# Performance work log

Measured on AMD Instinct MI355X. Metric: run time of the kernel, lower is better.

## Reference

```python
import jax, jax.numpy as jnp
import numpy as np

B, IN_SIZE, IN_DIM = 16, 2048, 512
HEADS, OUT_SIZE = 4, 64
EPS = 0.1
MAX_ITER = 30
SIGMA = 0.1


def setup_inputs() -> dict:
    key = jax.random.key(0)
    k1, k2 = jax.random.split(key)
    x = jax.random.normal(k1, (B, IN_SIZE, IN_DIM), dtype=jnp.float32)
    stdv = 1.0 / np.sqrt(OUT_SIZE)
    weight = jax.random.uniform(k2, (HEADS, OUT_SIZE, IN_DIM), jnp.float32, -stdv, stdv)
    return {"x": x, "weight": weight}


def _position_filter(in_size, out_size, sigma):
    # 1-D gaussian position filter (image=False branch of get_position_filter)
    a = jnp.arange(0.0, in_size, dtype=jnp.float32)[:, None] / in_size
    b = jnp.arange(0.0, out_size, dtype=jnp.float32)[None, :] / out_size
    return jnp.exp(-(((a - b) / sigma) ** 2))  # (in_size, out_size)


def log_sinkhorn(K, iterations):
    """Log-domain Sinkhorn. K: (B, H, N, M) log-kernel.
    Row marginal a = 1/N (uniform, no mask). Scaling vectors are
    detached (envelope trick) before forming the transport plan,
    matching the original OTK implementation."""
    Bn, H, N, M = K.shape
    log_a = jnp.full((Bn, H, N), -jnp.log(jnp.float32(N)), dtype=K.dtype)
    u0 = jnp.zeros((Bn, H, N), K.dtype)
    v0 = jnp.zeros((Bn, H, M), K.dtype)

    def step(carry, _):
        u, v = carry
        Z = K + u[..., :, None] + v[..., None, :]
        u = log_a - jax.nn.logsumexp(Z, axis=-1)
        Z = K + u[..., :, None] + v[..., None, :]
        v = -jax.nn.logsumexp(Z, axis=-2)
        return (u, v), None

    (u, v), _ = jax.lax.scan(step, (u0, v0), None, length=iterations)
    u = jax.lax.stop_gradient(u)
    v = jax.lax.stop_gradient(v)
    return jnp.exp(K + u[..., :, None] + v[..., None, :])  # (B,H,N,M)


def reference(x, weight):
    # x: (B, N, D); weight: (H, M, D)
    pf = _position_filter(IN_SIZE, OUT_SIZE, SIGMA)  # (N, M)
    # euclidean cost via expansion (cdist)
    x2 = jnp.sum(x * x, axis=-1)                      # (B, N)
    w2 = jnp.sum(weight * weight, axis=-1)            # (H, M)
    xw = jnp.einsum('bnd,hmd->bhnm', x, weight)       # (B, H, N, M)
    C = jnp.sqrt(jnp.maximum(x2[:, None, :, None] + w2[None, :, None, :] - 2.0 * xw, 0.0))
    K = (-C / EPS) * pf[None, None]                   # position filter applied to log-kernel
    P = log_sinkhorn(K, MAX_ITER)                     # (B, H, N, M) transport plan
    # attn: (B, M, H, N) -> (B, M*H, N)
    attn = jnp.transpose(P, (0, 3, 1, 2)).reshape(B, OUT_SIZE * HEADS, IN_SIZE)
    out = jnp.matmul(attn, x)                         # (B, M*H, D)
    return out.reshape(B, OUT_SIZE, HEADS * IN_DIM)
```

## Files before the change

### kernel.cpp

```cpp
#include <hip/hip_runtime.h>
#include <hip/hip_fp16.h>


typedef _Float16 h2 __attribute__((ext_vector_type(2)));
typedef _Float16 h8 __attribute__((ext_vector_type(8)));
typedef float f4 __attribute__((ext_vector_type(4)));

#define NB 16
#define NN 2048
#define ND 512
#define NH 4
#define NM 64
#define NITER 30
#define EUSCALE 8.0f

static __device__ __forceinline__ float fdot2f(h2 a, h2 b, float c) {
#if __has_builtin(__builtin_amdgcn_fdot2)
  return __builtin_amdgcn_fdot2(a, b, c, false);
#else
  return (float)a[0] * (float)b[0] + (float)a[1] * (float)b[1] + c;
#endif
}

static __device__ __forceinline__ h2 pkrtz(float a, float b) {
  return __builtin_bit_cast(h2, __builtin_amdgcn_cvt_pkrtz(a, b));
}

static __device__ __forceinline__ h8 pack8(float4 a, float4 b) {
  h8 r;
  r[0] = (_Float16)a.x; r[1] = (_Float16)a.y; r[2] = (_Float16)a.z; r[3] = (_Float16)a.w;
  r[4] = (_Float16)b.x; r[5] = (_Float16)b.y; r[6] = (_Float16)b.z; r[7] = (_Float16)b.w;
  return r;
}

static __device__ __forceinline__ float sq4(float4 a) {
  return a.x * a.x + a.y * a.y + a.z * a.z + a.w * a.w;
}

__global__ __launch_bounds__(256) void k0_xt(const float* __restrict__ x,
                                             _Float16* __restrict__ xT) {
  __shared__ float tile[64][65];
  const int b = blockIdx.z;
  const int n0 = blockIdx.x * 64;
  const int d0 = blockIdx.y * 64;
  const int t = threadIdx.x;
  const int nr = t >> 2;
  const int ds = (t & 3) * 16;
  const float4* src = (const float4*)(x + ((size_t)(b * NN + n0 + nr) * ND + d0 + ds));
  float4 v0 = src[0], v1 = src[1], v2 = src[2], v3 = src[3];
  float vals[16] = {v0.x, v0.y, v0.z, v0.w, v1.x, v1.y, v1.z, v1.w,
                    v2.x, v2.y, v2.z, v2.w, v3.x, v3.y, v3.z, v3.w};
#pragma unroll
  for (int j = 0; j < 16; ++j) tile[ds + j][nr] = vals[j];
  __syncthreads();
  const int dr = t >> 2;
  const int ns = (t & 3) * 16;
  h8 o0, o1;
#pragma unroll
  for (int j = 0; j < 8; ++j) o0[j] = (_Float16)tile[dr][ns + j];
#pragma unroll
  for (int j = 0; j < 8; ++j) o1[j] = (_Float16)tile[dr][ns + 8 + j];
  _Float16* dst = xT + ((size_t)(b * ND + d0 + dr) * NN + n0 + ns);
  *(h8*)dst = o0;
  *(h8*)(dst + 8) = o1;
}

__global__ __launch_bounds__(512) void k1_buildE(const float* __restrict__ x,
                                                 const float* __restrict__ w,
                                                 _Float16* __restrict__ E) {
  __shared__ _Float16 Ah[128][72];
  __shared__ _Float16 Bh[256][72];
  __shared__ float x2s[128][4];
  __shared__ float w2s[256][2];
  __shared__ float x2r[128];
  __shared__ float w2r[256];

  const int b = blockIdx.y;
  const int n0 = blockIdx.x * 128;
  const int tid = threadIdx.x;
  const int lane = tid & 63;
  const int wv = tid >> 6;
  const int lrow = lane & 15;
  const int kq = lane >> 4;

  f4 acc[16];
#pragma unroll
  for (int i = 0; i < 16; ++i) acc[i] = (f4){0.f, 0.f, 0.f, 0.f};

  const int ar = tid >> 2, ac = (tid & 3) * 16;
  const int br = tid >> 1, bc = (tid & 1) * 32;
  const float* xsrc = x + ((size_t)(b * NN + n0 + ar) * ND + ac);
  const float* wsrc = w + ((size_t)br * ND + bc);
  float x2p = 0.f, w2p = 0.f;

  for (int kt = 0; kt < 8; ++kt) {
    {
      const float4* s4 = (const float4*)(xsrc + kt * 64);
      float4 a0 = s4[0], a1 = s4[1], a2 = s4[2], a3 = s4[3];
      x2p += sq4(a0) + sq4(a1) + sq4(a2) + sq4(a3);
      *(h8*)&Ah[ar][ac] = pack8(a0, a1);
      *(h8*)&Ah[ar][ac + 8] = pack8(a2, a3);
    }
    {
      const float4* s4 = (const float4*)(wsrc + kt * 64);
      float4 u0 = s4[0], u1 = s4[1], u2 = s4[2], u3 = s4[3];
      float4 u4 = s4[4], u5 = s4[5], u6 = s4[6], u7 = s4[7];
      w2p += sq4(u0) + sq4(u1) + sq4(u2) + sq4(u3)
           + sq4(u4) + sq4(u5) + sq4(u6) + sq4(u7);
      *(h8*)&Bh[br][bc] = pack8(u0, u1);
      *(h8*)&Bh[br][bc + 8] = pack8(u2, u3);
      *(h8*)&Bh[br][bc + 16] = pack8(u4, u5);
      *(h8*)&Bh[br][bc + 24] = pack8(u6, u7);
    }
    __syncthreads();
#pragma unroll
    for (int s = 0; s < 2; ++s) {
      h8 af = *(const h8*)&Ah[wv * 16 + lrow][s * 32 + kq * 8];
#pragma unroll
      for (int cf = 0; cf < 16; ++cf) {
        h8 bf = *(const h8*)&Bh[cf * 16 + lrow][s * 32 + kq * 8];
        acc[cf] = __builtin_amdgcn_mfma_f32_16x16x32_f16(af, bf, acc[cf], 0, 0, 0);
      }
    }
    __syncthreads();
  }

  x2s[ar][tid & 3] = x2p;
  w2s[br][tid & 1] = w2p;
  __syncthreads();
  if (tid < 128) {
    x2r[tid] = x2s[tid][0] + x2s[tid][1] + x2s[tid][2] + x2s[tid][3];
  } else if (tid < 384) {
    const int r = tid - 128;
    w2r[r] = w2s[r][0] + w2s[r][1];
  }
  __syncthreads();

#pragma unroll
  for (int cf = 0; cf < 16; ++cf) {
    const int mg = cf * 16 + lrow;
    const int hh = mg >> 6;
    const int m = mg & 63;
    const float w2v = w2r[mg];
    const float bm = (float)m * (1.0f / 64.0f);
    _Float16* Eb = E + ((size_t)(b * NH + hh) * NN) * NM;
#pragma unroll
    for (int j = 0; j < 4; ++j) {
      const int nl = wv * 16 + kq * 4 + j;
      const int n = n0 + nl;
      const float c2 = x2r[nl] + w2v - 2.0f * acc[cf][j];
      const float Cd = sqrtf(fmaxf(c2, 0.0f));
      const float tt = (float)n * (1.0f / 2048.0f) - bm;
      const float pf = __expf(-100.0f * tt * tt);
      const float Ev = __expf(-10.0f * Cd * pf);
      Eb[(size_t)n * NM + m] = (_Float16)Ev;
    }
  }
}

__global__ __launch_bounds__(1024) void k2_sinkhorn(const _Float16* __restrict__ E,
                                                    _Float16* __restrict__ Pt) {
  const int bh = blockIdx.x;
  const int b = bh >> 2, h = bh & 3;
  const int tid = threadIdx.x;
  const int lane = tid & 63;

  __shared__ float evf[64];
  __shared__ __align__(16) h2 evh[32];
  __shared__ unsigned int pbuf[1024];

  const _Float16* Ep = E + (size_t)bh * (NN * NM);

  h2 e[2][32];
#pragma unroll
  for (int i = 0; i < 2; ++i) {
    const uint4* src = (const uint4*)(Ep + (size_t)(2 * tid + i) * NM);
#pragma unroll
    for (int q = 0; q < 8; ++q) {
      uint4 v = src[q];
      e[i][q * 4 + 0] = __builtin_bit_cast(h2, v.x);
      e[i][q * 4 + 1] = __builtin_bit_cast(h2, v.y);
      e[i][q * 4 + 2] = __builtin_bit_cast(h2, v.z);
      e[i][q * 4 + 3] = __builtin_bit_cast(h2, v.w);
    }
  }

  float eu[2] = {1.f, 1.f};
  if (tid < 64) evf[tid] = 1.f;
  if (tid < 32) evh[tid] = pkrtz(1.f, 1.f);
  __syncthreads();

#pragma unroll 1
  for (int it = 0; it < NITER; ++it) {
    h2 evr[32];
    {
      const uint4* ev4 = (const uint4*)evh;
#pragma unroll
      for (int q8 = 0; q8 < 8; ++q8) {
        uint4 v = ev4[q8];
        evr[q8 * 4 + 0] = __builtin_bit_cast(h2, v.x);
        evr[q8 * 4 + 1] = __builtin_bit_cast(h2, v.y);
        evr[q8 * 4 + 2] = __builtin_bit_cast(h2, v.z);
        evr[q8 * 4 + 3] = __builtin_bit_cast(h2, v.w);
      }
    }
    float s0a = 0.f, s0b = 0.f, s1a = 0.f, s1b = 0.f;
#pragma unroll
    for (int q = 0; q < 16; ++q) {
      s0a = fdot2f(e[0][q], evr[q], s0a);
      s1a = fdot2f(e[1][q], evr[q], s1a);
    }
#pragma unroll
    for (int q = 16; q < 32; ++q) {
      s0b = fdot2f(e[0][q], evr[q], s0b);
      s1b = fdot2f(e[1][q], evr[q], s1b);
    }
    eu[0] = 4.8828125e-4f * __builtin_amdgcn_rcpf(eu[0] * (s0a + s0b));
    eu[1] = 4.8828125e-4f * __builtin_amdgcn_rcpf(eu[1] * (s1a + s1b));
    const float es0 = eu[0] * EUSCALE, es1 = eu[1] * EUSCALE;
    const h2 eup0 = pkrtz(es0, es0);
    const h2 eup1 = pkrtz(es1, es1);
    h2 tp[32];
#pragma unroll
    for (int q = 0; q < 32; ++q) {
      tp[q] = e[0][q] * eup0 + e[1][q] * eup1;
    }
#pragma unroll
    for (int k = 0; k < 5; ++k) {
      const int nn = 32 >> k;
      const bool up = (lane >> k) & 1;
#pragma unroll
      for (int p = 0; p < (nn >> 1); ++p) {
        h2 keep = up ? tp[p + (nn >> 1)] : tp[p];
        h2 send = up ? tp[p] : tp[p + (nn >> 1)];
        int rv = __shfl_xor(__builtin_bit_cast(int, send), 1 << k, 64);
        tp[p] = keep + __builtin_bit_cast(h2, rv);
      }
    }
    pbuf[tid] = __builtin_bit_cast(unsigned int, tp[0]);
    __syncthreads();
    if (tid < 32) {
      const int j = tid;
      const int rev = ((j & 1) << 4) | ((j & 2) << 2) | (j & 4) | ((j & 8) >> 2) | ((j & 16) >> 4);
      float T0 = 0.f, T1 = 0.f;
#pragma unroll
      for (int wq = 0; wq < 16; ++wq) {
        h2 a = __builtin_bit_cast(h2, pbuf[wq * 64 + rev]);
        h2 c = __builtin_bit_cast(h2, pbuf[wq * 64 + rev + 32]);
        T0 += (float)a[0] + (float)c[0];
        T1 += (float)a[1] + (float)c[1];
      }
      const float e0 = evf[2 * j], e1 = evf[2 * j + 1];
      const float n0 = EUSCALE * __builtin_amdgcn_rcpf(e0 * T0);
      const float n1 = EUSCALE * __builtin_amdgcn_rcpf(e1 * T1);
      evf[2 * j] = n0;
      evf[2 * j + 1] = n1;
      evh[j] = pkrtz(n0, n1);
    }
    __syncthreads();
  }

  _Float16* Pb = Pt + ((size_t)(b * 256 + h)) * NN;
#pragma unroll
  for (int q = 0; q < 32; ++q) {
    const float ev0 = evf[2 * q];
    const float ev1 = evf[2 * q + 1];
    const float a00 = (float)e[0][q][0] * eu[0] * ev0;
    const float a10 = (float)e[1][q][0] * eu[1] * ev0;
    const float a01 = (float)e[0][q][1] * eu[0] * ev1;
    const float a11 = (float)e[1][q][1] * eu[1] * ev1;
    *(h2*)(Pb + (size_t)(2 * q) * 4 * NN + 2 * tid) = pkrtz(a00, a10);
    *(h2*)(Pb + (size_t)(2 * q + 1) * 4 * NN + 2 * tid) = pkrtz(a01, a11);
  }
}

__global__ __launch_bounds__(512) void k3_out(const _Float16* __restrict__ Pt,
                                              const _Float16* __restrict__ xT,
                                              float* __restrict__ out) {
  __shared__ _Float16 As[128][72];
  __shared__ _Float16 Bs[64][72];
  const int b = blockIdx.z;
  const int hf = blockIdx.y;
  const int dt = blockIdx.x;
  const int tid = threadIdx.x;
  const int lane = tid & 63;
  const int wv = tid >> 6;
  const int lrow = lane & 15;
  const int kq = lane >> 4;

  f4 acc[4];
#pragma unroll
  for (int i = 0; i < 4; ++i) acc[i] = (f4){0.f, 0.f, 0.f, 0.f};

  const int ar = tid >> 2, ac = (tid & 3) * 16;
  const int brd = tid >> 3, bn = (tid & 7) * 8;
  const _Float16* asrc = Pt + ((size_t)(b * 256 + hf * 128 + ar) * NN + ac);
  const _Float16* bsrc = xT + ((size_t)(b * ND + dt * 64 + brd) * NN + bn);

  for (int kt = 0; kt < 32; ++kt) {
    const int k0 = kt * 64;
    h8 a0 = *(const h8*)(asrc + k0);
    h8 a1 = *(const h8*)(asrc + k0 + 8);
    h8 bv = *(const h8*)(bsrc + k0);
    *(h8*)&As[ar][ac] = a0;
    *(h8*)&As[ar][ac + 8] = a1;
    *(h8*)&Bs[brd][bn] = bv;
    __syncthreads();
#pragma unroll
    for (int s = 0; s < 2; ++s) {
      h8 af = *(const h8*)&As[wv * 16 + lrow][s * 32 + kq * 8];
#pragma unroll
      for (int cf = 0; cf < 4; ++cf) {
        h8 bf = *(const h8*)&Bs[cf * 16 + lrow][s * 32 + kq * 8];
        acc[cf] = __builtin_amdgcn_mfma_f32_16x16x32_f16(af, bf, acc[cf], 0, 0, 0);
      }
    }
    __syncthreads();
  }
#pragma unroll
  for (int cf = 0; cf < 4; ++cf) {
    const int d = dt * 64 + cf * 16 + lrow;
#pragma unroll
    for (int j = 0; j < 4; ++j) {
      const int row = hf * 128 + wv * 16 + kq * 4 + j;
      out[(size_t)(b * 256 + row) * ND + d] = acc[cf][j];
    }
  }
}

extern "C" void kernel_launch(void* const* d_in, const int* in_sizes, int n_in,
                              void* d_out, int out_size, void* d_ws, size_t ws_size,
                              hipStream_t stream) {
  const float* x = (const float*)d_in[0];
  const float* w = (const float*)d_in[1];
  float* out = (float*)d_out;
  char* ws = (char*)d_ws;
  _Float16* xT = (_Float16*)ws;
  _Float16* E  = (_Float16*)(ws + (size_t)33554432);
  _Float16* Pt = (_Float16*)(ws + (size_t)50331648);

  k0_xt<<<dim3(32, 8, NB), 256, 0, stream>>>(x, xT);
  k1_buildE<<<dim3(16, NB), 512, 0, stream>>>(x, w, E);
  k2_sinkhorn<<<dim3(64), 1024, 0, stream>>>(E, Pt);
  k3_out<<<dim3(8, 2, NB), 512, 0, stream>>>(Pt, xT, out);
}
```

Before: 184.5 us.

## Halve sinkhorn block to 512 threads with four register-pinned rows each

The Sinkhorn kernel now runs 512 threads per block, each holding four rows of E (128 packed half2 registers) instead of two, and all storage is in named scalars pinned with empty asm so it stays in VGPRs. Column partial sums are combined over 8 waves instead of 16, and the epilogue writes 8-byte stores. This cuts cross-wave reduction and shuffle traffic per row, but raises register pressure and gives less latency hiding per block.

After: 178.1 us. 1.04x faster.

```diff
diff --git a/kernel.cpp b/kernel.cpp
--- a/kernel.cpp
+++ b/kernel.cpp
@@ -158,8 +158,23 @@
   }
 }
 
-__global__ __launch_bounds__(1024) void k2_sinkhorn(const _Float16* __restrict__ E,
-                                                    _Float16* __restrict__ Pt) {
+#define H2C(v, c) __builtin_bit_cast(h2, (v).c)
+#define EH(i, j, c) __builtin_bit_cast(h2, E##i##_##j##c)
+
+#define E_LIST(X) \
+  X(0,0) X(0,1) X(0,2) X(0,3) X(0,4) X(0,5) X(0,6) X(0,7) \
+  X(1,0) X(1,1) X(1,2) X(1,3) X(1,4) X(1,5) X(1,6) X(1,7) \
+  X(2,0) X(2,1) X(2,2) X(2,3) X(2,4) X(2,5) X(2,6) X(2,7) \
+  X(3,0) X(3,1) X(3,2) X(3,3) X(3,4) X(3,5) X(3,6) X(3,7)
+
+#define TP_LIST(X) \
+  X(0,0,x)  X(1,0,y)  X(2,0,z)  X(3,0,w)  X(4,1,x)  X(5,1,y)  X(6,1,z)  X(7,1,w) \
+  X(8,2,x)  X(9,2,y)  X(10,2,z) X(11,2,w) X(12,3,x) X(13,3,y) X(14,3,z) X(15,3,w) \
+  X(16,4,x) X(17,4,y) X(18,4,z) X(19,4,w) X(20,5,x) X(21,5,y) X(22,5,z) X(23,5,w) \
+  X(24,6,x) X(25,6,y) X(26,6,z) X(27,6,w) X(28,7,x) X(29,7,y) X(30,7,z) X(31,7,w)
+
+__global__ __launch_bounds__(512, 2) void k2_sinkhorn(const _Float16* __restrict__ E,
+                                                      _Float16* __restrict__ Pt) {
   const int bh = blockIdx.x;
   const int b = bh >> 2, h = bh & 3;
   const int tid = threadIdx.x;
@@ -167,84 +182,91 @@
 
   __shared__ float evf[64];
   __shared__ __align__(16) h2 evh[32];
-  __shared__ unsigned int pbuf[1024];
+  __shared__ unsigned int pbuf[512];
 
   const _Float16* Ep = E + (size_t)bh * (NN * NM);
-
-  h2 e[2][32];
-#pragma unroll
-  for (int i = 0; i < 2; ++i) {
-    const uint4* src = (const uint4*)(Ep + (size_t)(2 * tid + i) * NM);
-#pragma unroll
-    for (int q = 0; q < 8; ++q) {
-      uint4 v = src[q];
-      e[i][q * 4 + 0] = __builtin_bit_cast(h2, v.x);
-      e[i][q * 4 + 1] = __builtin_bit_cast(h2, v.y);
-      e[i][q * 4 + 2] = __builtin_bit_cast(h2, v.z);
-      e[i][q * 4 + 3] = __builtin_bit_cast(h2, v.w);
-    }
-  }
-
-  float eu[2] = {1.f, 1.f};
+  const uint4* s0 = (const uint4*)(Ep + (size_t)(4 * tid + 0) * NM);
+  const uint4* s1 = (const uint4*)(Ep + (size_t)(4 * tid + 1) * NM);
+  const uint4* s2 = (const uint4*)(Ep + (size_t)(4 * tid + 2) * NM);
+  const uint4* s3 = (const uint4*)(Ep + (size_t)(4 * tid + 3) * NM);
+
+#define DECLE(i, j) \
+  uint4 v##i##_##j = s##i[j]; \
+  unsigned int E##i##_##j##x = v##i##_##j.x; \
+  unsigned int E##i##_##j##y = v##i##_##j.y; \
+  unsigned int E##i##_##j##z = v##i##_##j.z; \
+  unsigned int E##i##_##j##w = v##i##_##j.w;
+  E_LIST(DECLE)
+#undef DECLE
+#define PINE(i, j) \
+  asm volatile("" : "+v"(E##i##_##j##x), "+v"(E##i##_##j##y), \
+                    "+v"(E##i##_##j##z), "+v"(E##i##_##j##w));
+  E_LIST(PINE)
+#undef PINE
+
+  float eu0 = 1.f, eu1 = 1.f, eu2 = 1.f, eu3 = 1.f;
   if (tid < 64) evf[tid] = 1.f;
   if (tid < 32) evh[tid] = pkrtz(1.f, 1.f);
   __syncthreads();
 
 #pragma unroll 1
   for (int it = 0; it < NITER; ++it) {
-    h2 evr[32];
-    {
-      const uint4* ev4 = (const uint4*)evh;
-#pragma unroll
-      for (int q8 = 0; q8 < 8; ++q8) {
-        uint4 v = ev4[q8];
-        evr[q8 * 4 + 0] = __builtin_bit_cast(h2, v.x);
-        evr[q8 * 4 + 1] = __builtin_bit_cast(h2, v.y);
-        evr[q8 * 4 + 2] = __builtin_bit_cast(h2, v.z);
-        evr[q8 * 4 + 3] = __builtin_bit_cast(h2, v.w);
-      }
-    }
-    float s0a = 0.f, s0b = 0.f, s1a = 0.f, s1b = 0.f;
-#pragma unroll
-    for (int q = 0; q < 16; ++q) {
-      s0a = fdot2f(e[0][q], evr[q], s0a);
-      s1a = fdot2f(e[1][q], evr[q], s1a);
-    }
-#pragma unroll
-    for (int q = 16; q < 32; ++q) {
-      s0b = fdot2f(e[0][q], evr[q], s0b);
-      s1b = fdot2f(e[1][q], evr[q], s1b);
-    }
-    eu[0] = 4.8828125e-4f * __builtin_amdgcn_rcpf(eu[0] * (s0a + s0b));
-    eu[1] = 4.8828125e-4f * __builtin_amdgcn_rcpf(eu[1] * (s1a + s1b));
-    const float es0 = eu[0] * EUSCALE, es1 = eu[1] * EUSCALE;
-    const h2 eup0 = pkrtz(es0, es0);
-    const h2 eup1 = pkrtz(es1, es1);
-    h2 tp[32];
-#pragma unroll
-    for (int q = 0; q < 32; ++q) {
-      tp[q] = e[0][q] * eup0 + e[1][q] * eup1;
-    }
-#pragma unroll
-    for (int k = 0; k < 5; ++k) {
-      const int nn = 32 >> k;
-      const bool up = (lane >> k) & 1;
-#pragma unroll
-      for (int p = 0; p < (nn >> 1); ++p) {
-        h2 keep = up ? tp[p + (nn >> 1)] : tp[p];
-        h2 send = up ? tp[p] : tp[p + (nn >> 1)];
-        int rv = __shfl_xor(__builtin_bit_cast(int, send), 1 << k, 64);
-        tp[p] = keep + __builtin_bit_cast(h2, rv);
-      }
-    }
-    pbuf[tid] = __builtin_bit_cast(unsigned int, tp[0]);
+    const uint4* ev4 = (const uint4*)evh;
+    uint4 V0 = ev4[0], V1 = ev4[1], V2 = ev4[2], V3 = ev4[3];
+    uint4 V4 = ev4[4], V5 = ev4[5], V6 = ev4[6], V7 = ev4[7];
+
+    float a0 = 0.f, b0 = 0.f, a1 = 0.f, b1 = 0.f;
+    float a2 = 0.f, b2 = 0.f, a3 = 0.f, b3 = 0.f;
+#define UP(i, j, acc) \
+    acc = fdot2f(EH(i, j, x), H2C(V##j, x), acc); \
+    acc = fdot2f(EH(i, j, y), H2C(V##j, y), acc); \
+    acc = fdot2f(EH(i, j, z), H2C(V##j, z), acc); \
+    acc = fdot2f(EH(i, j, w), H2C(V##j, w), acc);
+    UP(0,0,a0) UP(0,1,a0) UP(0,2,a0) UP(0,3,a0) UP(0,4,b0) UP(0,5,b0) UP(0,6,b0) UP(0,7,b0)
+    UP(1,0,a1) UP(1,1,a1) UP(1,2,a1) UP(1,3,a1) UP(1,4,b1) UP(1,5,b1) UP(1,6,b1) UP(1,7,b1)
+    UP(2,0,a2) UP(2,1,a2) UP(2,2,a2) UP(2,3,a2) UP(2,4,b2) UP(2,5,b2) UP(2,6,b2) UP(2,7,b2)
+    UP(3,0,a3) UP(3,1,a3) UP(3,2,a3) UP(3,3,a3) UP(3,4,b3) UP(3,5,b3) UP(3,6,b3) UP(3,7,b3)
+#undef UP
+    eu0 = 4.8828125e-4f * __builtin_amdgcn_rcpf(eu0 * (a0 + b0));
+    eu1 = 4.8828125e-4f * __builtin_amdgcn_rcpf(eu1 * (a1 + b1));
+    eu2 = 4.8828125e-4f * __builtin_amdgcn_rcpf(eu2 * (a2 + b2));
+    eu3 = 4.8828125e-4f * __builtin_amdgcn_rcpf(eu3 * (a3 + b3));
+
+    const h2 p0 = pkrtz(eu0 * EUSCALE, eu0 * EUSCALE);
+    const h2 p1 = pkrtz(eu1 * EUSCALE, eu1 * EUSCALE);
+    const h2 p2 = pkrtz(eu2 * EUSCALE, eu2 * EUSCALE);
+    const h2 p3 = pkrtz(eu3 * EUSCALE, eu3 * EUSCALE);
+#define DECLT(q, j, c) \
+    h2 t##q = EH(0, j, c) * p0 + EH(1, j, c) * p1 + \
+              EH(2, j, c) * p2 + EH(3, j, c) * p3;
+    TP_LIST(DECLT)
+#undef DECLT
+
+    const bool up0 = lane & 1, up1 = (lane >> 1) & 1, up2 = (lane >> 2) & 1;
+    const bool up3 = (lane >> 3) & 1, up4 = (lane >> 4) & 1;
+#define BF(k, A, B) { \
+    h2 keep_ = up##k ? B : A; \
+    h2 send_ = up##k ? A : B; \
+    int rv_ = __shfl_xor(__builtin_bit_cast(int, send_), 1 << k, 64); \
+    A = keep_ + __builtin_bit_cast(h2, rv_); }
+    BF(0,t0,t16) BF(0,t1,t17) BF(0,t2,t18)  BF(0,t3,t19)
+    BF(0,t4,t20) BF(0,t5,t21) BF(0,t6,t22)  BF(0,t7,t23)
+    BF(0,t8,t24) BF(0,t9,t25) BF(0,t10,t26) BF(0,t11,t27)
+    BF(0,t12,t28) BF(0,t13,t29) BF(0,t14,t30) BF(0,t15,t31)
+    BF(1,t0,t8)  BF(1,t1,t9)  BF(1,t2,t10) BF(1,t3,t11)
+    BF(1,t4,t12) BF(1,t5,t13) BF(1,t6,t14) BF(1,t7,t15)
+    BF(2,t0,t4)  BF(2,t1,t5)  BF(2,t2,t6)  BF(2,t3,t7)
+    BF(3,t0,t2)  BF(3,t1,t3)
+    BF(4,t0,t1)
+#undef BF
+    pbuf[tid] = __builtin_bit_cast(unsigned int, t0);
     __syncthreads();
     if (tid < 32) {
       const int j = tid;
       const int rev = ((j & 1) << 4) | ((j & 2) << 2) | (j & 4) | ((j & 8) >> 2) | ((j & 16) >> 4);
       float T0 = 0.f, T1 = 0.f;
 #pragma unroll
-      for (int wq = 0; wq < 16; ++wq) {
+      for (int wq = 0; wq < 8; ++wq) {
         h2 a = __builtin_bit_cast(h2, pbuf[wq * 64 + rev]);
         h2 c = __builtin_bit_cast(h2, pbuf[wq * 64 + rev + 32]);
         T0 += (float)a[0] + (float)c[0];
@@ -261,17 +283,20 @@
   }
 
   _Float16* Pb = Pt + ((size_t)(b * 256 + h)) * NN;
-#pragma unroll
-  for (int q = 0; q < 32; ++q) {
-    const float ev0 = evf[2 * q];
-    const float ev1 = evf[2 * q + 1];
-    const float a00 = (float)e[0][q][0] * eu[0] * ev0;
-    const float a10 = (float)e[1][q][0] * eu[1] * ev0;
-    const float a01 = (float)e[0][q][1] * eu[0] * ev1;
-    const float a11 = (float)e[1][q][1] * eu[1] * ev1;
-    *(h2*)(Pb + (size_t)(2 * q) * 4 * NN + 2 * tid) = pkrtz(a00, a10);
-    *(h2*)(Pb + (size_t)(2 * q + 1) * 4 * NN + 2 * tid) = pkrtz(a01, a11);
-  }
+#define EPI(q, j, c) { \
+    const float ev0_ = evf[2 * (q)]; \
+    const float ev1_ = evf[2 * (q) + 1]; \
+    const h2 x0_ = EH(0, j, c), x1_ = EH(1, j, c); \
+    const h2 x2_ = EH(2, j, c), x3_ = EH(3, j, c); \
+    uint2 st0_, st1_; \
+    st0_.x = __builtin_bit_cast(unsigned int, pkrtz((float)x0_[0] * eu0 * ev0_, (float)x1_[0] * eu1 * ev0_)); \
+    st0_.y = __builtin_bit_cast(unsigned int, pkrtz((float)x2_[0] * eu2 * ev0_, (float)x3_[0] * eu3 * ev0_)); \
+    st1_.x = __builtin_bit_cast(unsigned int, pkrtz((float)x0_[1] * eu0 * ev1_, (float)x1_[1] * eu1 * ev1_)); \
+    st1_.y = __builtin_bit_cast(unsigned int, pkrtz((float)x2_[1] * eu2 * ev1_, (float)x3_[1] * eu3 * ev1_)); \
+    *(uint2*)(Pb + (size_t)(2 * (q)) * 4 * NN + 4 * tid) = st0_; \
+    *(uint2*)(Pb + (size_t)(2 * (q) + 1) * 4 * NN + 4 * tid) = st1_; }
+  TP_LIST(EPI)
+#undef EPI
 }
 
 __global__ __launch_bounds__(512) void k3_out(const _Float16* __restrict__ Pt,
@@ -341,6 +366,6 @@
 
   k0_xt<<<dim3(32, 8, NB), 256, 0, stream>>>(x, xT);
   k1_buildE<<<dim3(16, NB), 512, 0, stream>>>(x, w, E);
-  k2_sinkhorn<<<dim3(64), 1024, 0, stream>>>(E, Pt);
+  k2_sinkhorn<<<dim3(64), 512, 0, stream>>>(E, Pt);
   k3_out<<<dim3(8, 2, NB), 512, 0, stream>>>(Pt, xT, out);
 }
```
